# Optimization experiments

Hardware: AMD Instinct MI355X
Metric: run time of the kernel (lower is better)

Reference implementation:

```python
import jax, jax.numpy as jnp
import numpy as np

B, L, DH = 8, 4096, 1024
T, DG, P = 1024, 768, 256
EPS = 1e-8


def setup_inputs() -> dict:
    key = jax.random.key(0)
    k1, k2, k3, k4 = jax.random.split(key, 4)
    H = jax.random.normal(k1, (B, L, DH), dtype=jnp.float32)
    G = jax.random.normal(k2, (B, T, DG), dtype=jnp.float32)
    # nn.Linear(d, P, bias=False) weights: shape [P, d], uniform(-1/sqrt(d), 1/sqrt(d))
    Wq = jax.random.uniform(k3, (P, DG), jnp.float32, -1.0, 1.0) / jnp.sqrt(jnp.float32(DG))
    Wk = jax.random.uniform(k4, (P, DH), jnp.float32, -1.0, 1.0) / jnp.sqrt(jnp.float32(DH))
    return {"H": H, "G": G, "Wq": Wq, "Wk": Wk}


def reference(H, G, Wq, Wk):
    # Chunked online-softmax streaming is mathematically equivalent to one
    # full stable softmax cross-attention pass; values are the raw H.
    scale = jnp.float32(P) ** -0.5
    Q = jnp.einsum("btd,pd->btp", G, Wq)          # [B,T,P]
    K = jnp.einsum("bld,pd->blp", H, Wk)          # [B,L,P]
    logits = jnp.einsum("btp,blp->btl", Q, K).astype(jnp.float32) * scale
    m = jnp.max(logits, axis=-1, keepdims=True)
    p = jnp.exp(logits - m)                        # [B,T,L]
    s = jnp.sum(p, axis=-1, keepdims=True)         # [B,T,1]
    z = jnp.einsum("btl,bld->btd", p, H.astype(jnp.float32))
    Z = (z / (s + EPS)).astype(H.dtype)            # [B,T,DH]
    return Z
```

## Files before the change

kernel.cpp:

```cpp
#include <hip/hip_runtime.h>
#include <hip/hip_bf16.h>
#include <stdint.h>

#define Bn  8
#define Ln  4096
#define DHn 1024
#define Tn  1024
#define DGn 768
#define Pn  256

typedef float  f32x4  __attribute__((ext_vector_type(4)));
typedef __bf16 bf16x8 __attribute__((ext_vector_type(8)));

__device__ __forceinline__ void gload16(const void* g, void* l) {
  __builtin_amdgcn_global_load_lds(
      (const __attribute__((address_space(1))) void*)g,
      (__attribute__((address_space(3))) void*)l, 16, 0, 0);
}

__device__ __forceinline__ unsigned short f2bf(float x) {
  union { float f; uint32_t u; } v; v.f = x;
  uint32_t u = v.u;
  return (unsigned short)((u + 0x7FFFu + ((u >> 16) & 1u)) >> 16);
}

__device__ __forceinline__ float bf2f(unsigned short b) {
  union { uint32_t u; float f; } v; v.u = ((uint32_t)b) << 16;
  return v.f;
}

__global__ void cvt_kernel(const float4* __restrict__ in,
                           ushort4* __restrict__ out, int n4) {
  int i = blockIdx.x * 256 + threadIdx.x;
  if (i < n4) {
    float4 v = in[i];
    ushort4 o;
    o.x = f2bf(v.x); o.y = f2bf(v.y); o.z = f2bf(v.z); o.w = f2bf(v.w);
    out[i] = o;
  }
}

__global__ void transpose_cvt(const float* __restrict__ Hg,
                              unsigned short* __restrict__ HT) {
  __shared__ unsigned short tile[64 * 65];
  const int b  = blockIdx.z;
  const int l0 = blockIdx.x * 64;
  const int d0 = blockIdx.y * 64;
  const float4* src = (const float4*)(Hg + (size_t)b * Ln * DHn);
  for (int e = threadIdx.x; e < 1024; e += 256) {
    int l  = e >> 4;
    int d4 = e & 15;
    float4 v = src[((size_t)(l0 + l) * DHn + d0) / 4 + d4];
    int d = d4 * 4;
    tile[(d + 0) * 65 + l] = f2bf(v.x);
    tile[(d + 1) * 65 + l] = f2bf(v.y);
    tile[(d + 2) * 65 + l] = f2bf(v.z);
    tile[(d + 3) * 65 + l] = f2bf(v.w);
  }
  __syncthreads();
  ushort4* dst = (ushort4*)(HT + (size_t)b * DHn * Ln);
  for (int e = threadIdx.x; e < 1024; e += 256) {
    int d  = e >> 4;
    int l4 = (e & 15) * 4;
    ushort4 o;
    o.x = tile[d * 65 + l4 + 0];
    o.y = tile[d * 65 + l4 + 1];
    o.z = tile[d * 65 + l4 + 2];
    o.w = tile[d * 65 + l4 + 3];
    dst[((size_t)(d0 + d) * Ln + l0) / 4 + (e & 15)] = o;
  }
}

template <int EPI>
__global__ __launch_bounds__(256) void gemm_bt(
    const unsigned short* __restrict__ A, const unsigned short* __restrict__ B,
    void* __restrict__ Cout, float* __restrict__ S,
    int K, int lda, int ldb, int ldc,
    long sA, long sB, long sC, int sS, float scale) {
  __shared__ unsigned short As[128 * 32];
  __shared__ unsigned short Bs[128 * 32];
  const int b = blockIdx.z;
  const unsigned short* Ab = A + (long)b * sA;
  const unsigned short* Bb = B + (long)b * sB;
  const int m0 = blockIdx.x * 128;
  const int n0 = blockIdx.y * 128;
  const int tid  = threadIdx.x;
  const int lane = tid & 63;
  const int wave = tid >> 6;
  const int wm = (wave >> 1) << 6;
  const int wn = (wave & 1) << 6;
  const int lrow = lane & 15;
  const int quad = lane >> 4;
  const int srow0 = lane >> 2;
  const int skcol = (lane & 3) << 3;

  f32x4 acc[4][4];
#pragma unroll
  for (int mt = 0; mt < 4; ++mt)
#pragma unroll
    for (int nt = 0; nt < 4; ++nt) acc[mt][nt] = f32x4{0.f, 0.f, 0.f, 0.f};

  for (int k0 = 0; k0 < K; k0 += 32) {
    __syncthreads();
#pragma unroll
    for (int j = 0; j < 2; ++j) {
      int c = wave * 2 + j;
      int row = c * 16 + srow0;
      gload16(Ab + (size_t)(m0 + row) * lda + (k0 + skcol), &As[c * 512]);
      gload16(Bb + (size_t)(n0 + row) * ldb + (k0 + skcol), &Bs[c * 512]);
    }
    __syncthreads();
    bf16x8 af[4], bfr[4];
#pragma unroll
    for (int mt = 0; mt < 4; ++mt)
      af[mt] = *(const bf16x8*)&As[(wm + mt * 16 + lrow) * 32 + quad * 8];
#pragma unroll
    for (int nt = 0; nt < 4; ++nt)
      bfr[nt] = *(const bf16x8*)&Bs[(wn + nt * 16 + lrow) * 32 + quad * 8];
#pragma unroll
    for (int mt = 0; mt < 4; ++mt)
#pragma unroll
      for (int nt = 0; nt < 4; ++nt)
        acc[mt][nt] = __builtin_amdgcn_mfma_f32_16x16x32_bf16(
            af[mt], bfr[nt], acc[mt][nt], 0, 0, 0);
  }

  if (EPI == 0) {
    unsigned short* C = (unsigned short*)Cout + (long)b * sC;
#pragma unroll
    for (int mt = 0; mt < 4; ++mt)
#pragma unroll
      for (int r = 0; r < 4; ++r) {
        int row = m0 + wm + mt * 16 + quad * 4 + r;
        unsigned short* Cr = C + (size_t)row * ldc + n0 + wn + lrow;
#pragma unroll
        for (int nt = 0; nt < 4; ++nt) Cr[nt * 16] = f2bf(acc[mt][nt][r]);
      }
  } else if (EPI == 1) {
    unsigned short* C = (unsigned short*)Cout + (long)b * sC;
    float* Sb = S + (long)b * sS;
#pragma unroll
    for (int mt = 0; mt < 4; ++mt)
#pragma unroll
      for (int r = 0; r < 4; ++r) {
        int row = m0 + wm + mt * 16 + quad * 4 + r;
        unsigned short* Cr = C + (size_t)row * ldc + n0 + wn + lrow;
        float psum = 0.f;
#pragma unroll
        for (int nt = 0; nt < 4; ++nt) {
          float e = __expf(acc[mt][nt][r] * scale);
          unsigned short bv = f2bf(e);
          Cr[nt * 16] = bv;
          psum += bf2f(bv);
        }
        psum += __shfl_xor(psum, 1);
        psum += __shfl_xor(psum, 2);
        psum += __shfl_xor(psum, 4);
        psum += __shfl_xor(psum, 8);
        if (lrow == 0) atomicAdd(&Sb[row], psum);
      }
  } else {
    float* C = (float*)Cout + (long)b * sC;
    const float* Sb = S + (long)b * sS;
#pragma unroll
    for (int mt = 0; mt < 4; ++mt)
#pragma unroll
      for (int r = 0; r < 4; ++r) {
        int row = m0 + wm + mt * 16 + quad * 4 + r;
        float inv = 1.f / (Sb[row] + 1e-8f);
        float* Cr = C + (size_t)row * ldc + n0 + wn + lrow;
#pragma unroll
        for (int nt = 0; nt < 4; ++nt) Cr[nt * 16] = acc[mt][nt][r] * inv;
      }
  }
}

extern "C" void kernel_launch(void* const* d_in, const int* in_sizes, int n_in,
                              void* d_out, int out_size, void* d_ws, size_t ws_size,
                              hipStream_t stream) {
  const float* H  = (const float*)d_in[0];
  const float* G  = (const float*)d_in[1];
  const float* Wq = (const float*)d_in[2];
  const float* Wk = (const float*)d_in[3];
  float* out = (float*)d_out;

  char* ws = (char*)d_ws;
  size_t off = 0;
  auto alloc = [&](size_t bytes) {
    void* p = ws + off;
    off = (off + bytes + 255) & ~(size_t)255;
    return p;
  };
  unsigned short* Hb  = (unsigned short*)alloc((size_t)Bn * Ln * DHn * 2);
  unsigned short* HbT = (unsigned short*)alloc((size_t)Bn * DHn * Ln * 2);
  unsigned short* Gb  = (unsigned short*)alloc((size_t)Bn * Tn * DGn * 2);
  unsigned short* Wqb = (unsigned short*)alloc((size_t)Pn * DGn * 2);
  unsigned short* Wkb = (unsigned short*)alloc((size_t)Pn * DHn * 2);
  unsigned short* Kb  = (unsigned short*)alloc((size_t)Bn * Ln * Pn * 2);
  unsigned short* Qb  = (unsigned short*)alloc((size_t)Bn * Tn * Pn * 2);
  float* Sv           = (float*)alloc((size_t)Bn * Tn * 4);
  unsigned short* Pm = Hb;

  {
    int n4 = Bn * Ln * DHn / 4;
    cvt_kernel<<<(n4 + 255) / 256, 256, 0, stream>>>((const float4*)H, (ushort4*)Hb, n4);
  }
  {
    int n4 = Bn * Tn * DGn / 4;
    cvt_kernel<<<(n4 + 255) / 256, 256, 0, stream>>>((const float4*)G, (ushort4*)Gb, n4);
  }
  {
    int n4 = Pn * DGn / 4;
    cvt_kernel<<<(n4 + 255) / 256, 256, 0, stream>>>((const float4*)Wq, (ushort4*)Wqb, n4);
  }
  {
    int n4 = Pn * DHn / 4;
    cvt_kernel<<<(n4 + 255) / 256, 256, 0, stream>>>((const float4*)Wk, (ushort4*)Wkb, n4);
  }
  transpose_cvt<<<dim3(Ln / 64, DHn / 64, Bn), 256, 0, stream>>>(H, HbT);
  hipMemsetAsync(Sv, 0, (size_t)Bn * Tn * 4, stream);

  gemm_bt<0><<<dim3(Ln / 128, Pn / 128, Bn), 256, 0, stream>>>(
      Hb, Wkb, Kb, nullptr, DHn, DHn, DHn, Pn,
      (long)Ln * DHn, 0L, (long)Ln * Pn, 0, 1.f);
  gemm_bt<0><<<dim3(Tn / 128, Pn / 128, Bn), 256, 0, stream>>>(
      Gb, Wqb, Qb, nullptr, DGn, DGn, DGn, Pn,
      (long)Tn * DGn, 0L, (long)Tn * Pn, 0, 1.f);
  gemm_bt<1><<<dim3(Tn / 128, Ln / 128, Bn), 256, 0, stream>>>(
      Qb, Kb, Pm, Sv, Pn, Pn, Pn, Ln,
      (long)Tn * Pn, (long)Ln * Pn, (long)Tn * Ln, Tn, 0.0625f);
  gemm_bt<2><<<dim3(Tn / 128, DHn / 128, Bn), 256, 0, stream>>>(
      Pm, HbT, out, Sv, Ln, Ln, Ln, DHn,
      (long)Tn * Ln, (long)DHn * Ln, (long)Tn * DHn, Tn, 1.f);
}
```

Before: 504.3 us.

## Fuse H conversion into transpose, batch-interleave tile grid, split-K final GEMM

```diff
diff --git a/kernel.cpp b/kernel.cpp
--- a/kernel.cpp
+++ b/kernel.cpp
@@ -40,22 +40,28 @@
   }
 }
 
-__global__ void transpose_cvt(const float* __restrict__ Hg,
-                              unsigned short* __restrict__ HT) {
+__global__ void prep_H(const float* __restrict__ Hg,
+                       unsigned short* __restrict__ Hb,
+                       unsigned short* __restrict__ HT) {
   __shared__ unsigned short tile[64 * 65];
   const int b  = blockIdx.z;
   const int l0 = blockIdx.x * 64;
   const int d0 = blockIdx.y * 64;
-  const float4* src = (const float4*)(Hg + (size_t)b * Ln * DHn);
+  const float4* src  = (const float4*)(Hg + (size_t)b * Ln * DHn);
+  ushort4*      dstH = (ushort4*)(Hb + (size_t)b * Ln * DHn);
   for (int e = threadIdx.x; e < 1024; e += 256) {
     int l  = e >> 4;
     int d4 = e & 15;
-    float4 v = src[((size_t)(l0 + l) * DHn + d0) / 4 + d4];
+    size_t idx4 = ((size_t)(l0 + l) * DHn + d0) / 4 + d4;
+    float4 v = src[idx4];
+    ushort4 o;
+    o.x = f2bf(v.x); o.y = f2bf(v.y); o.z = f2bf(v.z); o.w = f2bf(v.w);
+    dstH[idx4] = o;
     int d = d4 * 4;
-    tile[(d + 0) * 65 + l] = f2bf(v.x);
-    tile[(d + 1) * 65 + l] = f2bf(v.y);
-    tile[(d + 2) * 65 + l] = f2bf(v.z);
-    tile[(d + 3) * 65 + l] = f2bf(v.w);
+    tile[(d + 0) * 65 + l] = o.x;
+    tile[(d + 1) * 65 + l] = o.y;
+    tile[(d + 2) * 65 + l] = o.z;
+    tile[(d + 3) * 65 + l] = o.w;
   }
   __syncthreads();
   ushort4* dst = (ushort4*)(HT + (size_t)b * DHn * Ln);
@@ -75,15 +81,21 @@
 __global__ __launch_bounds__(256) void gemm_bt(
     const unsigned short* __restrict__ A, const unsigned short* __restrict__ B,
     void* __restrict__ Cout, float* __restrict__ S,
-    int K, int lda, int ldb, int ldc,
-    long sA, long sB, long sC, int sS, float scale) {
+    int kLen, int lda, int ldb, int ldc,
+    long sA, long sB, long sC, int sS, float scale, int mTiles, int nTiles) {
   __shared__ unsigned short As[128 * 32];
   __shared__ unsigned short Bs[128 * 32];
-  const int b = blockIdx.z;
+  int x = blockIdx.x;
+  const int b = x & (Bn - 1);
+  int r = x >> 3;
+  const int ni = r % nTiles; r /= nTiles;
+  const int mi = r % mTiles;
+  const int ks = r / mTiles;
   const unsigned short* Ab = A + (long)b * sA;
   const unsigned short* Bb = B + (long)b * sB;
-  const int m0 = blockIdx.x * 128;
-  const int n0 = blockIdx.y * 128;
+  const int m0 = mi * 128;
+  const int n0 = ni * 128;
+  const int kBeg = ks * kLen;
   const int tid  = threadIdx.x;
   const int lane = tid & 63;
   const int wave = tid >> 6;
@@ -100,7 +112,7 @@
 #pragma unroll
     for (int nt = 0; nt < 4; ++nt) acc[mt][nt] = f32x4{0.f, 0.f, 0.f, 0.f};
 
-  for (int k0 = 0; k0 < K; k0 += 32) {
+  for (int k0 = kBeg; k0 < kBeg + kLen; k0 += 32) {
     __syncthreads();
 #pragma unroll
     for (int j = 0; j < 2; ++j) {
@@ -130,11 +142,11 @@
 #pragma unroll
     for (int mt = 0; mt < 4; ++mt)
 #pragma unroll
-      for (int r = 0; r < 4; ++r) {
-        int row = m0 + wm + mt * 16 + quad * 4 + r;
+      for (int r2 = 0; r2 < 4; ++r2) {
+        int row = m0 + wm + mt * 16 + quad * 4 + r2;
         unsigned short* Cr = C + (size_t)row * ldc + n0 + wn + lrow;
 #pragma unroll
-        for (int nt = 0; nt < 4; ++nt) Cr[nt * 16] = f2bf(acc[mt][nt][r]);
+        for (int nt = 0; nt < 4; ++nt) Cr[nt * 16] = f2bf(acc[mt][nt][r2]);
       }
   } else if (EPI == 1) {
     unsigned short* C = (unsigned short*)Cout + (long)b * sC;
@@ -142,13 +154,13 @@
 #pragma unroll
     for (int mt = 0; mt < 4; ++mt)
 #pragma unroll
-      for (int r = 0; r < 4; ++r) {
-        int row = m0 + wm + mt * 16 + quad * 4 + r;
+      for (int r2 = 0; r2 < 4; ++r2) {
+        int row = m0 + wm + mt * 16 + quad * 4 + r2;
         unsigned short* Cr = C + (size_t)row * ldc + n0 + wn + lrow;
         float psum = 0.f;
 #pragma unroll
         for (int nt = 0; nt < 4; ++nt) {
-          float e = __expf(acc[mt][nt][r] * scale);
+          float e = __expf(acc[mt][nt][r2] * scale);
           unsigned short bv = f2bf(e);
           Cr[nt * 16] = bv;
           psum += bf2f(bv);
@@ -165,12 +177,15 @@
 #pragma unroll
     for (int mt = 0; mt < 4; ++mt)
 #pragma unroll
-      for (int r = 0; r < 4; ++r) {
-        int row = m0 + wm + mt * 16 + quad * 4 + r;
+      for (int r2 = 0; r2 < 4; ++r2) {
+        int row = m0 + wm + mt * 16 + quad * 4 + r2;
         float inv = 1.f / (Sb[row] + 1e-8f);
         float* Cr = C + (size_t)row * ldc + n0 + wn + lrow;
 #pragma unroll
-        for (int nt = 0; nt < 4; ++nt) Cr[nt * 16] = acc[mt][nt][r] * inv;
+        for (int nt = 0; nt < 4; ++nt) {
+          if (EPI == 2) Cr[nt * 16] = acc[mt][nt][r2] * inv;
+          else          atomicAdd(&Cr[nt * 16], acc[mt][nt][r2] * inv);
+        }
       }
   }
 }
@@ -202,10 +217,6 @@
   unsigned short* Pm = Hb;
 
   {
-    int n4 = Bn * Ln * DHn / 4;
-    cvt_kernel<<<(n4 + 255) / 256, 256, 0, stream>>>((const float4*)H, (ushort4*)Hb, n4);
-  }
-  {
     int n4 = Bn * Tn * DGn / 4;
     cvt_kernel<<<(n4 + 255) / 256, 256, 0, stream>>>((const float4*)G, (ushort4*)Gb, n4);
   }
@@ -217,19 +228,20 @@
     int n4 = Pn * DHn / 4;
     cvt_kernel<<<(n4 + 255) / 256, 256, 0, stream>>>((const float4*)Wk, (ushort4*)Wkb, n4);
   }
-  transpose_cvt<<<dim3(Ln / 64, DHn / 64, Bn), 256, 0, stream>>>(H, HbT);
+  prep_H<<<dim3(Ln / 64, DHn / 64, Bn), 256, 0, stream>>>(H, Hb, HbT);
   hipMemsetAsync(Sv, 0, (size_t)Bn * Tn * 4, stream);
-
-  gemm_bt<0><<<dim3(Ln / 128, Pn / 128, Bn), 256, 0, stream>>>(
+  hipMemsetAsync(out, 0, (size_t)Bn * Tn * DHn * 4, stream);
+
+  gemm_bt<0><<<Bn * 32 * 2, 256, 0, stream>>>(
       Hb, Wkb, Kb, nullptr, DHn, DHn, DHn, Pn,
-      (long)Ln * DHn, 0L, (long)Ln * Pn, 0, 1.f);
-  gemm_bt<0><<<dim3(Tn / 128, Pn / 128, Bn), 256, 0, stream>>>(
+      (long)Ln * DHn, 0L, (long)Ln * Pn, 0, 1.f, 32, 2);
+  gemm_bt<0><<<Bn * 8 * 2, 256, 0, stream>>>(
       Gb, Wqb, Qb, nullptr, DGn, DGn, DGn, Pn,
-      (long)Tn * DGn, 0L, (long)Tn * Pn, 0, 1.f);
-  gemm_bt<1><<<dim3(Tn / 128, Ln / 128, Bn), 256, 0, stream>>>(
+      (long)Tn * DGn, 0L, (long)Tn * Pn, 0, 1.f, 8, 2);
+  gemm_bt<1><<<Bn * 8 * 32, 256, 0, stream>>>(
       Qb, Kb, Pm, Sv, Pn, Pn, Pn, Ln,
-      (long)Tn * Pn, (long)Ln * Pn, (long)Tn * Ln, Tn, 0.0625f);
-  gemm_bt<2><<<dim3(Tn / 128, DHn / 128, Bn), 256, 0, stream>>>(
-      Pm, HbT, out, Sv, Ln, Ln, Ln, DHn,
-      (long)Tn * Ln, (long)DHn * Ln, (long)Tn * DHn, Tn, 1.f);
-}
+      (long)Tn * Pn, (long)Ln * Pn, (long)Tn * Ln, Tn, 0.0625f, 8, 32);
+  gemm_bt<3><<<Bn * 8 * 8 * 2, 256, 0, stream>>>(
+      Pm, HbT, out, Sv, Ln / 2, Ln, Ln, DHn,
+      (long)Tn * Ln, (long)DHn * Ln, (long)Tn * DHn, Tn, 1.f, 8, 8);
+}
```

After: 507.5 us. Within noise of the previous version (+0.6%).
